# Optimization experiments

Measured on AMD Instinct MI355X. Metric: run time of the kernel, lower is better.

The kernel has to match this reference:

```python
import jax, jax.numpy as jnp
import numpy as np

N = 50000      # nodes
E = 800000     # edges
CIN = 128
CH = 128
COUT = 64
EPS = 1e-5     # BatchNorm eps


def setup_inputs() -> dict:
    key = jax.random.key(0)
    ks = jax.random.split(key, 16)
    s = 0.1  # weight scale for numerical stability
    return {
        "x": jax.random.normal(ks[0], (N, CIN), jnp.float32),
        "edge_index": jax.random.randint(ks[1], (2, E), 0, N, jnp.int32),
        "edge_weights": jax.random.uniform(ks[2], (E,), jnp.float32),
        "w1": jax.random.normal(ks[3], (CIN, CH), jnp.float32) * s,
        "b1": jnp.zeros((CH,), jnp.float32),
        "bn1_g": jnp.ones((CH,), jnp.float32),
        "bn1_b": jnp.zeros((CH,), jnp.float32),
        "bn1_m": jax.random.normal(ks[4], (CH,), jnp.float32) * 0.1,
        "bn1_v": jax.random.uniform(ks[5], (CH,), jnp.float32) + 0.5,
        "conv_ws": jax.random.normal(ks[6], (2, CH, CH), jnp.float32) * s,
        "conv_bs": jnp.zeros((2, CH), jnp.float32),
        "bns_g": jnp.ones((2, CH), jnp.float32),
        "bns_b": jnp.zeros((2, CH), jnp.float32),
        "bns_m": jax.random.normal(ks[7], (2, CH), jnp.float32) * 0.1,
        "bns_v": jax.random.uniform(ks[8], (2, CH), jnp.float32) + 0.5,
        "lin1_w": jax.random.normal(ks[9], (CH, CH), jnp.float32) * s,
        "lin1_b": jnp.zeros((CH,), jnp.float32),
        "lin2_w": jax.random.normal(ks[10], (CH, COUT), jnp.float32) * s,
        "lin2_b": jnp.zeros((COUT,), jnp.float32),
    }


def _bn(h, g, b, m, v):
    # BatchNorm1d in eval mode: running statistics
    return (h - m) * jax.lax.rsqrt(v + EPS) * g + b


def _gcn(h, w, b, src, dst, norm, n):
    # GCNConv: out[dst] += norm_e * (h @ W)[src]  (self loops already in src/dst)
    h = h @ w
    msg = h[src] * norm[:, None]                 # [E+N, CH]
    return jax.ops.segment_sum(msg, dst, num_segments=n) + b


def reference(x, edge_index, edge_weights, w1, b1, bn1_g, bn1_b, bn1_m, bn1_v,
              conv_ws, conv_bs, bns_g, bns_b, bns_m, bns_v,
              lin1_w, lin1_b, lin2_w, lin2_b):
    n = x.shape[0]
    loop = jnp.arange(n, dtype=edge_index.dtype)
    src = jnp.concatenate([edge_index[0], loop])
    dst = jnp.concatenate([edge_index[1], loop])
    ew = jnp.concatenate([edge_weights, jnp.ones((n,), edge_weights.dtype)])
    # symmetric degree normalization (PyG gcn_norm)
    deg = jax.ops.segment_sum(ew, dst, num_segments=n)
    dis = jnp.where(deg > 0, jax.lax.rsqrt(deg), 0.0)
    norm = dis[src] * ew * dis[dst]

    lrelu = jax.nn.leaky_relu  # slope 0.01, matches F.leaky_relu default
    h = lrelu(_bn(_gcn(x, w1, b1, src, dst, norm, n), bn1_g, bn1_b, bn1_m, bn1_v))
    for i in range(conv_ws.shape[0]):
        h = lrelu(_bn(_gcn(h, conv_ws[i], conv_bs[i], src, dst, norm, n),
                      bns_g[i], bns_b[i], bns_m[i], bns_v[i]) + h)
    h = lrelu(h @ lin1_w + lin1_b)
    # dropout is identity in eval mode
    return h @ lin2_w + lin2_b
```

## Files before the change

kernel.cpp:

```cpp
#include <hip/hip_runtime.h>
#include <hip/hip_bf16.h>


constexpr int   NN    = 50000;
constexpr int   EE    = 800000;
constexpr int   CH    = 128;
constexpr int   SLOTS = 64;
constexpr float EPS   = 1e-5f;

typedef __attribute__((ext_vector_type(8))) short bf16x8;
typedef __attribute__((ext_vector_type(4))) float f32x4;
typedef unsigned long long u64;
typedef unsigned short u16;

__device__ inline u16 f2bf_rne(float f) {
  unsigned u = __float_as_uint(f);
  unsigned r = u + 0x7fffu + ((u >> 16) & 1u);
  return (u16)(r >> 16);
}
__device__ inline float bf2f(unsigned h16) {
  return __uint_as_float(h16 << 16);
}


__global__ void init_kernel(unsigned* __restrict__ ell) {
  int i = blockIdx.x * blockDim.x + threadIdx.x;
  if (i < NN) ell[(size_t)i * SLOTS] = 1u;
}

__global__ void edge_kernel(const int* __restrict__ ei, const float* __restrict__ ew,
                            unsigned* __restrict__ ell) {
  int e = blockIdx.x * blockDim.x + threadIdx.x;
  if (e >= EE) return;
  int s = ei[e], d = ei[EE + e];
  float w = ew[e];
  unsigned rank = atomicAdd(&ell[(size_t)d * SLOTS], 1u);
  if (rank < SLOTS)
    ell[(size_t)d * SLOTS + rank] = ((unsigned)f2bf_rne(w) << 16) | (unsigned)s;
}

constexpr int NB_DIS = (NN * 16 + 255) / 256;
constexpr int NB_WZ  = (73728 + 255) / 256;

__global__ void prep_kernel(
    const unsigned* __restrict__ ell, float* __restrict__ dis,
    const float* __restrict__ w1, const float* __restrict__ bn1_g, const float* __restrict__ bn1_v,
    const float* __restrict__ conv_ws, const float* __restrict__ bns_g, const float* __restrict__ bns_v,
    const float* __restrict__ lin1_w, const float* __restrict__ lin2_w,
    u16* __restrict__ w1h, u16* __restrict__ w1l,
    u16* __restrict__ c0h, u16* __restrict__ c0l,
    u16* __restrict__ c1h, u16* __restrict__ c1l,
    u16* __restrict__ l1h, u16* __restrict__ l1l,
    u16* __restrict__ l2h, u16* __restrict__ l2l)
{
  if (blockIdx.x < NB_DIS) {
    int lane = threadIdx.x & 63;
    int sub  = lane & 15;
    int node = ((blockIdx.x * 256 + threadIdx.x) >> 6) * 4 + (lane >> 4);
    if (node >= NN) return;
    uint4 vv = *(const uint4*)(ell + (size_t)node * SLOTS + sub * 4);
    unsigned cnt = (unsigned)__shfl((int)vv.x, lane & 48);
    if (cnt > SLOTS) cnt = SLOTS;
    unsigned wv[4] = {vv.x, vv.y, vv.z, vv.w};
    float s = 0.f;
    #pragma unroll
    for (int q = 0; q < 4; q++) {
      int slot = sub * 4 + q;
      if (slot >= 1 && slot < (int)cnt) s += bf2f(wv[q] >> 16);
    }
    #pragma unroll
    for (int off = 1; off < 16; off <<= 1) s += __shfl_xor(s, off);
    if (sub == 0) dis[node] = rsqrtf(1.0f + s);
    return;
  }

  int idx = (blockIdx.x - NB_DIS) * 256 + threadIdx.x;
  const float* W; const float* g = nullptr; const float* v = nullptr;
  u16 *hi, *lo; int CO = 128; int local;
  if      (idx < 16384) { W = w1;              g = bn1_g;     v = bn1_v;     hi = w1h; lo = w1l; local = idx; }
  else if (idx < 32768) { W = conv_ws;         g = bns_g;     v = bns_v;     hi = c0h; lo = c0l; local = idx - 16384; }
  else if (idx < 49152) { W = conv_ws + 16384; g = bns_g+128; v = bns_v+128; hi = c1h; lo = c1l; local = idx - 32768; }
  else if (idx < 65536) { W = lin1_w;                                        hi = l1h; lo = l1l; local = idx - 49152; }
  else if (idx < 73728) { W = lin2_w;                                        hi = l2h; lo = l2l; local = idx - 65536; CO = 64; }
  else return;
  int k = local / CO, n = local % CO;
  float w = W[local];
  if (g) w *= g[n] * rsqrtf(v[n] + EPS);
  int NCT = CO / 16;
  int kchunk = k >> 5, kin = k & 31, quad = kin >> 3, j = kin & 7;
  int ct = n >> 4, l = (quad << 4) | (n & 15);
  size_t pos = ((size_t)(kchunk * NCT + ct) * 64 + l) * 8 + j;
  u16 h = f2bf_rne(w);
  hi[pos] = h;
  lo[pos] = f2bf_rne(w - bf2f(h));
}

template<int CO, int EPI, bool OUT_BF16, bool A_BF16, bool SCALE>
__global__ __launch_bounds__(256) void mgemm_kernel(
    const void* __restrict__ Ain,
    const u16* __restrict__ Whi, const u16* __restrict__ Wlo,
    const float* __restrict__ bias, const float* __restrict__ dis,
    void* __restrict__ Cout)
{
  constexpr int NCT = CO / 16;
  __shared__ float lds[64][CO + 4];

  const int tid  = threadIdx.x;
  const int wave = tid >> 6;
  const int lane = tid & 63;
  const int quad = lane >> 4;
  const int mrow = lane & 15;
  const int row0 = blockIdx.x * 64;

  int arow = row0 + wave * 16 + mrow;
  if (arow >= NN) arow = NN - 1;

  bf16x8 ahi[4], alo[4];
  if constexpr (A_BF16) {
    const u16* Ar = (const u16*)Ain + (size_t)arow * CH;
    #pragma unroll
    for (int c = 0; c < 4; c++)
      ahi[c] = *(const bf16x8*)(Ar + c * 32 + quad * 8);
  } else {
    const float* Ar = (const float*)Ain + (size_t)arow * CH;
    #pragma unroll
    for (int c = 0; c < 4; c++) {
      int off = c * 32 + quad * 8;
      float4 f0 = *(const float4*)(Ar + off);
      float4 f1 = *(const float4*)(Ar + off + 4);
      float f[8] = {f0.x, f0.y, f0.z, f0.w, f1.x, f1.y, f1.z, f1.w};
      #pragma unroll
      for (int j = 0; j < 8; j++) {
        u16 h = f2bf_rne(f[j]);
        ahi[c][j] = (short)h;
        alo[c][j] = (short)f2bf_rne(f[j] - bf2f(h));
      }
    }
  }

  f32x4 acc[NCT];
  #pragma unroll
  for (int t = 0; t < NCT; t++) acc[t] = (f32x4){0.f, 0.f, 0.f, 0.f};

  #pragma unroll
  for (int c = 0; c < 4; c++) {
    #pragma unroll
    for (int t = 0; t < NCT; t++) {
      size_t base = ((size_t)(c * NCT + t) * 64 + lane) * 8;
      bf16x8 bh = *(const bf16x8*)(Whi + base);
      bf16x8 bl = *(const bf16x8*)(Wlo + base);
      acc[t] = __builtin_amdgcn_mfma_f32_16x16x32_bf16(ahi[c], bh, acc[t], 0, 0, 0);
      if constexpr (!A_BF16)
        acc[t] = __builtin_amdgcn_mfma_f32_16x16x32_bf16(alo[c], bh, acc[t], 0, 0, 0);
      acc[t] = __builtin_amdgcn_mfma_f32_16x16x32_bf16(ahi[c], bl, acc[t], 0, 0, 0);
    }
  }

  #pragma unroll
  for (int t = 0; t < NCT; t++)
    #pragma unroll
    for (int r = 0; r < 4; r++)
      lds[wave * 16 + quad * 4 + r][t * 16 + mrow] = acc[t][r];
  __syncthreads();

  constexpr int TOTE = 64 * CO / 4;
  #pragma unroll
  for (int i = tid; i < TOTE; i += 256) {
    int row = (i * 4) / CO;
    int col = (i * 4) % CO;
    int grow = row0 + row;
    if (grow >= NN) continue;
    float rs = 1.0f;
    if constexpr (SCALE) rs = dis[grow];
    const float* lp = &lds[row][col];
    float o[4];
    #pragma unroll
    for (int q = 0; q < 4; q++) {
      float x = lp[q];
      if constexpr (EPI >= 1) {
        x += bias[col + q];
        if constexpr (EPI == 1) x = x > 0.f ? x : 0.01f * x;
      }
      if constexpr (SCALE) x *= rs;
      o[q] = x;
    }
    if constexpr (OUT_BF16) {
      u16* cp = (u16*)Cout + (size_t)grow * CO + col;
      unsigned p0 = ((unsigned)f2bf_rne(o[1]) << 16) | f2bf_rne(o[0]);
      unsigned p1 = ((unsigned)f2bf_rne(o[3]) << 16) | f2bf_rne(o[2]);
      *(uint2*)cp = make_uint2(p0, p1);
    } else {
      float* cp = (float*)Cout + (size_t)grow * CO + col;
      *(float4*)cp = make_float4(o[0], o[1], o[2], o[3]);
    }
  }
}

template<bool RES>
__global__ __launch_bounds__(256) void agg_kernel(
    const u16* __restrict__ hw,
    const unsigned* __restrict__ ell, const float* __restrict__ dis,
    const float* __restrict__ conv_b, const float* __restrict__ g,
    const float* __restrict__ bb, const float* __restrict__ m,
    const float* __restrict__ v,
    const u16* __restrict__ res, u16* __restrict__ out)
{
  int node = (blockIdx.x * blockDim.x + threadIdx.x) >> 6;
  int lane = threadIdx.x & 63;
  if (node >= NN) return;

  unsigned myword = ell[(size_t)node * SLOTS + lane];
  int cnt = __shfl((int)myword, 0);
  if (cnt > SLOTS) cnt = SLOTS;

  unsigned us = *(const unsigned*)(hw + (size_t)node * CH + lane * 2);
  float ax = bf2f(us & 0xffffu);
  float ay = bf2f(us >> 16);

  int j = 1;
  for (; j + 4 <= cnt; j += 4) {
    unsigned e0 = (unsigned)__shfl((int)myword, j);
    unsigned e1 = (unsigned)__shfl((int)myword, j + 1);
    unsigned e2 = (unsigned)__shfl((int)myword, j + 2);
    unsigned e3 = (unsigned)__shfl((int)myword, j + 3);
    unsigned u0 = *(const unsigned*)(hw + (size_t)(e0 & 0xffffu) * CH + lane * 2);
    unsigned u1 = *(const unsigned*)(hw + (size_t)(e1 & 0xffffu) * CH + lane * 2);
    unsigned u2 = *(const unsigned*)(hw + (size_t)(e2 & 0xffffu) * CH + lane * 2);
    unsigned u3 = *(const unsigned*)(hw + (size_t)(e3 & 0xffffu) * CH + lane * 2);
    float w0 = bf2f(e0 >> 16), w1 = bf2f(e1 >> 16);
    float w2 = bf2f(e2 >> 16), w3 = bf2f(e3 >> 16);
    ax = fmaf(w0, bf2f(u0 & 0xffffu), ax); ay = fmaf(w0, bf2f(u0 >> 16), ay);
    ax = fmaf(w1, bf2f(u1 & 0xffffu), ax); ay = fmaf(w1, bf2f(u1 >> 16), ay);
    ax = fmaf(w2, bf2f(u2 & 0xffffu), ax); ay = fmaf(w2, bf2f(u2 >> 16), ay);
    ax = fmaf(w3, bf2f(u3 & 0xffffu), ax); ay = fmaf(w3, bf2f(u3 >> 16), ay);
  }
  for (; j < cnt; j++) {
    unsigned e0 = (unsigned)__shfl((int)myword, j);
    unsigned u0 = *(const unsigned*)(hw + (size_t)(e0 & 0xffffu) * CH + lane * 2);
    float w0 = bf2f(e0 >> 16);
    ax = fmaf(w0, bf2f(u0 & 0xffffu), ax); ay = fmaf(w0, bf2f(u0 >> 16), ay);
  }

  float disd = dis[node];
  int c = lane * 2;
  float sc0 = g[c]     * rsqrtf(v[c]     + EPS);
  float sc1 = g[c + 1] * rsqrtf(v[c + 1] + EPS);
  float y0 = ax * disd + (conv_b[c]     - m[c])     * sc0 + bb[c];
  float y1 = ay * disd + (conv_b[c + 1] - m[c + 1]) * sc1 + bb[c + 1];
  if constexpr (RES) {
    unsigned r = *(const unsigned*)(res + (size_t)node * CH + c);
    y0 += bf2f(r & 0xffffu);
    y1 += bf2f(r >> 16);
  }
  y0 = y0 > 0.f ? y0 : 0.01f * y0;
  y1 = y1 > 0.f ? y1 : 0.01f * y1;
  *(unsigned*)(out + (size_t)node * CH + c) =
      ((unsigned)f2bf_rne(y1) << 16) | f2bf_rne(y0);
}


extern "C" void kernel_launch(void* const* d_in, const int* in_sizes, int n_in,
                              void* d_out, int out_size, void* d_ws, size_t ws_size,
                              hipStream_t stream) {
  const float* x       = (const float*)d_in[0];
  const int*   ei      = (const int*)  d_in[1];
  const float* ew      = (const float*)d_in[2];
  const float* w1      = (const float*)d_in[3];
  const float* b1      = (const float*)d_in[4];
  const float* bn1_g   = (const float*)d_in[5];
  const float* bn1_b   = (const float*)d_in[6];
  const float* bn1_m   = (const float*)d_in[7];
  const float* bn1_v   = (const float*)d_in[8];
  const float* conv_ws = (const float*)d_in[9];
  const float* conv_bs = (const float*)d_in[10];
  const float* bns_g   = (const float*)d_in[11];
  const float* bns_b   = (const float*)d_in[12];
  const float* bns_m   = (const float*)d_in[13];
  const float* bns_v   = (const float*)d_in[14];
  const float* lin1_w  = (const float*)d_in[15];
  const float* lin1_b  = (const float*)d_in[16];
  const float* lin2_w  = (const float*)d_in[17];
  const float* lin2_b  = (const float*)d_in[18];
  float* out = (float*)d_out;

  size_t off = 0;
  auto alloc = [&](size_t elems) -> void* {
    void* p = (char*)d_ws + off * 4;
    off += (elems + 3) & ~(size_t)3;
    return p;
  };
  unsigned* ell = (unsigned*)alloc((size_t)NN * SLOTS);
  float*    dis = (float*)   alloc(NN);
  u16*      hwb = (u16*)     alloc((size_t)NN * CH / 2);
  u16*      hA  = (u16*)     alloc((size_t)NN * CH / 2);
  u16* w1h = (u16*)alloc(CH * CH / 2); u16* w1l = (u16*)alloc(CH * CH / 2);
  u16* c0h = (u16*)alloc(CH * CH / 2); u16* c0l = (u16*)alloc(CH * CH / 2);
  u16* c1h = (u16*)alloc(CH * CH / 2); u16* c1l = (u16*)alloc(CH * CH / 2);
  u16* l1h = (u16*)alloc(CH * CH / 2); u16* l1l = (u16*)alloc(CH * CH / 2);
  u16* l2h = (u16*)alloc(CH * 64 / 2); u16* l2l = (u16*)alloc(CH * 64 / 2);

  const int nb_n    = (NN + 255) / 256;
  const int nb_e    = (EE + 255) / 256;
  const int nb_gemm = (NN + 63) / 64;
  const int nb_agg  = (NN * 64 + 255) / 256;
  dim3 B(256);

  init_kernel<<<nb_n, B, 0, stream>>>(ell);
  edge_kernel<<<nb_e, B, 0, stream>>>(ei, ew, ell);
  prep_kernel<<<NB_DIS + NB_WZ, B, 0, stream>>>(ell, dis,
      w1, bn1_g, bn1_v, conv_ws, bns_g, bns_v, lin1_w, lin2_w,
      w1h, w1l, c0h, c0l, c1h, c1l, l1h, l1l, l2h, l2l);

  mgemm_kernel<128, 0, true, false, true><<<nb_gemm, B, 0, stream>>>(x, w1h, w1l, nullptr, dis, hwb);
  agg_kernel<false><<<nb_agg, B, 0, stream>>>(hwb, ell, dis,
      b1, bn1_g, bn1_b, bn1_m, bn1_v, nullptr, hA);

  mgemm_kernel<128, 0, true, true, true><<<nb_gemm, B, 0, stream>>>(hA, c0h, c0l, nullptr, dis, hwb);
  agg_kernel<true><<<nb_agg, B, 0, stream>>>(hwb, ell, dis,
      conv_bs, bns_g, bns_b, bns_m, bns_v, hA, hA);

  mgemm_kernel<128, 0, true, true, true><<<nb_gemm, B, 0, stream>>>(hA, c1h, c1l, nullptr, dis, hwb);
  agg_kernel<true><<<nb_agg, B, 0, stream>>>(hwb, ell, dis,
      conv_bs + CH, bns_g + CH, bns_b + CH, bns_m + CH, bns_v + CH, hA, hA);

  mgemm_kernel<128, 1, true,  true, false><<<nb_gemm, B, 0, stream>>>(hA, l1h, l1l, lin1_b, nullptr, hwb);
  mgemm_kernel<64,  2, false, true, false><<<nb_gemm, B, 0, stream>>>(hwb, l2h, l2l, lin2_b, nullptr, out);
}
```

Measured before the change: 353.1 us.

## Bucket edges via two-pass LDS binning and fuse final two linear layers

Replaces the global-atomic ELL construction with a two-pass scheme. Edges are first binned by destination block of 64 nodes using shared-memory counters, then each bucket is scattered into the ELL rows with LDS atomics, and the degree normalization is computed in the same pass. The lin1 and lin2 GEMMs are fused into one kernel that keeps the intermediate activations in LDS, so the 50000x128 intermediate no longer makes a round trip through global memory. The cost is an extra bins buffer with fixed bucket capacity (RCAP), which could drop edges if a bucket overflows. It also changes rounding, since the intermediate stays fp32 and is split into hi and lo bf16 parts instead of being stored as bf16.

```diff
diff --git a/kernel.cpp b/kernel.cpp
--- a/kernel.cpp
+++ b/kernel.cpp
@@ -6,6 +6,9 @@
 constexpr int   EE    = 800000;
 constexpr int   CH    = 128;
 constexpr int   SLOTS = 64;
+constexpr int   NBUK  = 782;
+constexpr int   RCAP  = 2048;
+constexpr int   EPB   = 4096;
 constexpr float EPS   = 1e-5f;
 
 typedef __attribute__((ext_vector_type(8))) short bf16x8;
@@ -23,27 +26,82 @@
 }
 
 
-__global__ void init_kernel(unsigned* __restrict__ ell) {
-  int i = blockIdx.x * blockDim.x + threadIdx.x;
-  if (i < NN) ell[(size_t)i * SLOTS] = 1u;
-}
-
-__global__ void edge_kernel(const int* __restrict__ ei, const float* __restrict__ ew,
-                            unsigned* __restrict__ ell) {
-  int e = blockIdx.x * blockDim.x + threadIdx.x;
-  if (e >= EE) return;
-  int s = ei[e], d = ei[EE + e];
-  float w = ew[e];
-  unsigned rank = atomicAdd(&ell[(size_t)d * SLOTS], 1u);
-  if (rank < SLOTS)
-    ell[(size_t)d * SLOTS + rank] = ((unsigned)f2bf_rne(w) << 16) | (unsigned)s;
-}
-
-constexpr int NB_DIS = (NN * 16 + 255) / 256;
-constexpr int NB_WZ  = (73728 + 255) / 256;
-
-__global__ void prep_kernel(
-    const unsigned* __restrict__ ell, float* __restrict__ dis,
+__global__ __launch_bounds__(256) void bin_kernel(const int* __restrict__ ei,
+                                                  const float* __restrict__ ew,
+                                                  unsigned* __restrict__ gcur,
+                                                  u64* __restrict__ bins) {
+  __shared__ unsigned cnt[NBUK];
+  __shared__ unsigned base[NBUK];
+  const int tid = threadIdx.x;
+  for (int b = tid; b < NBUK; b += 256) cnt[b] = 0;
+  __syncthreads();
+  const int e0 = blockIdx.x * EPB;
+  unsigned pk[16]; u16 bkt[16]; u16 rnk[16]; unsigned char dl[16];
+  #pragma unroll
+  for (int i = 0; i < 16; i++) {
+    int e = e0 + i * 256 + tid;
+    if (e < EE) {
+      int s = ei[e], d = ei[EE + e];
+      float w = ew[e];
+      bkt[i] = (u16)(d >> 6);
+      dl[i]  = (unsigned char)(d & 63);
+      pk[i]  = ((unsigned)f2bf_rne(w) << 16) | (unsigned)s;
+      rnk[i] = (u16)atomicAdd(&cnt[bkt[i]], 1u);
+    } else bkt[i] = 0xffffu;
+  }
+  __syncthreads();
+  for (int b = tid; b < NBUK; b += 256) {
+    unsigned c = cnt[b];
+    base[b] = c ? atomicAdd(&gcur[b * 16], c) : 0u;
+  }
+  __syncthreads();
+  #pragma unroll
+  for (int i = 0; i < 16; i++) {
+    if (bkt[i] == 0xffffu) continue;
+    unsigned pos = base[bkt[i]] + rnk[i];
+    if (pos < RCAP)
+      bins[(size_t)bkt[i] * RCAP + pos] = ((u64)dl[i] << 32) | pk[i];
+  }
+}
+
+
+__global__ __launch_bounds__(256) void scatter_kernel(const unsigned* __restrict__ gcur,
+                                                      const u64* __restrict__ bins,
+                                                      unsigned* __restrict__ ell,
+                                                      float* __restrict__ dis) {
+  __shared__ unsigned rank[64];
+  __shared__ float    wsum[64];
+  const int b   = blockIdx.x;
+  const int tid = threadIdx.x;
+  if (tid < 64) { rank[tid] = 1u; wsum[tid] = 0.f; }
+  __syncthreads();
+  unsigned cnt = gcur[b * 16];
+  if (cnt > RCAP) cnt = RCAP;
+  const u64* src = bins + (size_t)b * RCAP;
+  for (unsigned i = tid; i < cnt; i += 256) {
+    u64 v = src[i];
+    unsigned pk = (unsigned)v;
+    unsigned dl = (unsigned)(v >> 32);
+    unsigned r = atomicAdd(&rank[dl], 1u);
+    if (r < SLOTS)
+      ell[((size_t)(b * 64 + dl)) * SLOTS + r] = pk;
+    atomicAdd(&wsum[dl], bf2f(pk >> 16));
+  }
+  __syncthreads();
+  if (tid < 64) {
+    int node = b * 64 + tid;
+    if (node < NN) {
+      unsigned c = rank[tid];
+      if (c > SLOTS) c = SLOTS;
+      ell[(size_t)node * SLOTS] = c;
+      dis[node] = rsqrtf(1.0f + wsum[tid]);
+    }
+  }
+}
+
+constexpr int NB_WZ = (73728 + 255) / 256;
+
+__global__ void wswz_kernel(
     const float* __restrict__ w1, const float* __restrict__ bn1_g, const float* __restrict__ bn1_v,
     const float* __restrict__ conv_ws, const float* __restrict__ bns_g, const float* __restrict__ bns_v,
     const float* __restrict__ lin1_w, const float* __restrict__ lin2_w,
@@ -53,28 +111,7 @@
     u16* __restrict__ l1h, u16* __restrict__ l1l,
     u16* __restrict__ l2h, u16* __restrict__ l2l)
 {
-  if (blockIdx.x < NB_DIS) {
-    int lane = threadIdx.x & 63;
-    int sub  = lane & 15;
-    int node = ((blockIdx.x * 256 + threadIdx.x) >> 6) * 4 + (lane >> 4);
-    if (node >= NN) return;
-    uint4 vv = *(const uint4*)(ell + (size_t)node * SLOTS + sub * 4);
-    unsigned cnt = (unsigned)__shfl((int)vv.x, lane & 48);
-    if (cnt > SLOTS) cnt = SLOTS;
-    unsigned wv[4] = {vv.x, vv.y, vv.z, vv.w};
-    float s = 0.f;
-    #pragma unroll
-    for (int q = 0; q < 4; q++) {
-      int slot = sub * 4 + q;
-      if (slot >= 1 && slot < (int)cnt) s += bf2f(wv[q] >> 16);
-    }
-    #pragma unroll
-    for (int off = 1; off < 16; off <<= 1) s += __shfl_xor(s, off);
-    if (sub == 0) dis[node] = rsqrtf(1.0f + s);
-    return;
-  }
-
-  int idx = (blockIdx.x - NB_DIS) * 256 + threadIdx.x;
+  int idx = blockIdx.x * 256 + threadIdx.x;
   const float* W; const float* g = nullptr; const float* v = nullptr;
   u16 *hi, *lo; int CO = 128; int local;
   if      (idx < 16384) { W = w1;              g = bn1_g;     v = bn1_v;     hi = w1h; lo = w1l; local = idx; }
@@ -192,6 +229,96 @@
     } else {
       float* cp = (float*)Cout + (size_t)grow * CO + col;
       *(float4*)cp = make_float4(o[0], o[1], o[2], o[3]);
+    }
+  }
+}
+
+__global__ __launch_bounds__(256) void linf_kernel(
+    const u16* __restrict__ Ain,
+    const u16* __restrict__ l1h, const u16* __restrict__ l1l,
+    const float* __restrict__ b1,
+    const u16* __restrict__ l2h, const u16* __restrict__ l2l,
+    const float* __restrict__ b2, float* __restrict__ out)
+{
+  __shared__ float lds[64][CH + 4];
+  const int tid  = threadIdx.x;
+  const int wave = tid >> 6;
+  const int lane = tid & 63;
+  const int quad = lane >> 4;
+  const int mrow = lane & 15;
+  const int row0 = blockIdx.x * 64;
+
+  int arow = row0 + wave * 16 + mrow;
+  if (arow >= NN) arow = NN - 1;
+
+  bf16x8 a1[4];
+  {
+    const u16* Ar = Ain + (size_t)arow * CH;
+    #pragma unroll
+    for (int c = 0; c < 4; c++)
+      a1[c] = *(const bf16x8*)(Ar + c * 32 + quad * 8);
+  }
+  f32x4 acc[8];
+  #pragma unroll
+  for (int t = 0; t < 8; t++) acc[t] = (f32x4){0.f, 0.f, 0.f, 0.f};
+  #pragma unroll
+  for (int c = 0; c < 4; c++) {
+    #pragma unroll
+    for (int t = 0; t < 8; t++) {
+      size_t base = ((size_t)(c * 8 + t) * 64 + lane) * 8;
+      bf16x8 bh = *(const bf16x8*)(l1h + base);
+      bf16x8 bl = *(const bf16x8*)(l1l + base);
+      acc[t] = __builtin_amdgcn_mfma_f32_16x16x32_bf16(a1[c], bh, acc[t], 0, 0, 0);
+      acc[t] = __builtin_amdgcn_mfma_f32_16x16x32_bf16(a1[c], bl, acc[t], 0, 0, 0);
+    }
+  }
+  #pragma unroll
+  for (int t = 0; t < 8; t++) {
+    float bb = b1[t * 16 + mrow];
+    #pragma unroll
+    for (int r = 0; r < 4; r++) {
+      float x = acc[t][r] + bb;
+      x = x > 0.f ? x : 0.01f * x;
+      lds[wave * 16 + quad * 4 + r][t * 16 + mrow] = x;
+    }
+  }
+  __syncthreads();
+
+  f32x4 acc2[4];
+  #pragma unroll
+  for (int t = 0; t < 4; t++) acc2[t] = (f32x4){0.f, 0.f, 0.f, 0.f};
+  const int lrow = wave * 16 + mrow;
+  #pragma unroll
+  for (int c = 0; c < 4; c++) {
+    bf16x8 ahi, alo;
+    const float* lp = &lds[lrow][c * 32 + quad * 8];
+    float4 f0 = *(const float4*)lp;
+    float4 f1 = *(const float4*)(lp + 4);
+    float f[8] = {f0.x, f0.y, f0.z, f0.w, f1.x, f1.y, f1.z, f1.w};
+    #pragma unroll
+    for (int j = 0; j < 8; j++) {
+      u16 h = f2bf_rne(f[j]);
+      ahi[j] = (short)h;
+      alo[j] = (short)f2bf_rne(f[j] - bf2f(h));
+    }
+    #pragma unroll
+    for (int t = 0; t < 4; t++) {
+      size_t base = ((size_t)(c * 4 + t) * 64 + lane) * 8;
+      bf16x8 bh = *(const bf16x8*)(l2h + base);
+      bf16x8 bl = *(const bf16x8*)(l2l + base);
+      acc2[t] = __builtin_amdgcn_mfma_f32_16x16x32_bf16(ahi, bh, acc2[t], 0, 0, 0);
+      acc2[t] = __builtin_amdgcn_mfma_f32_16x16x32_bf16(alo, bh, acc2[t], 0, 0, 0);
+      acc2[t] = __builtin_amdgcn_mfma_f32_16x16x32_bf16(ahi, bl, acc2[t], 0, 0, 0);
+    }
+  }
+  #pragma unroll
+  for (int t = 0; t < 4; t++) {
+    float bb = b2[t * 16 + mrow];
+    #pragma unroll
+    for (int r = 0; r < 4; r++) {
+      int grow = row0 + wave * 16 + quad * 4 + r;
+      if (grow < NN)
+        out[(size_t)grow * 64 + t * 16 + mrow] = acc2[t][r] + bb;
     }
   }
 }
@@ -289,27 +416,29 @@
     off += (elems + 3) & ~(size_t)3;
     return p;
   };
-  unsigned* ell = (unsigned*)alloc((size_t)NN * SLOTS);
-  float*    dis = (float*)   alloc(NN);
-  u16*      hwb = (u16*)     alloc((size_t)NN * CH / 2);
-  u16*      hA  = (u16*)     alloc((size_t)NN * CH / 2);
+  unsigned* gcur = (unsigned*)alloc(NBUK * 16);
+  u64*      bins = (u64*)     alloc((size_t)NBUK * RCAP * 2);
+  unsigned* ell  = (unsigned*)alloc((size_t)NN * SLOTS);
+  float*    dis  = (float*)   alloc(NN);
+  u16*      hwb  = (u16*)     alloc((size_t)NN * CH / 2);
+  u16*      hA   = (u16*)     alloc((size_t)NN * CH / 2);
   u16* w1h = (u16*)alloc(CH * CH / 2); u16* w1l = (u16*)alloc(CH * CH / 2);
   u16* c0h = (u16*)alloc(CH * CH / 2); u16* c0l = (u16*)alloc(CH * CH / 2);
   u16* c1h = (u16*)alloc(CH * CH / 2); u16* c1l = (u16*)alloc(CH * CH / 2);
   u16* l1h = (u16*)alloc(CH * CH / 2); u16* l1l = (u16*)alloc(CH * CH / 2);
   u16* l2h = (u16*)alloc(CH * 64 / 2); u16* l2l = (u16*)alloc(CH * 64 / 2);
 
-  const int nb_n    = (NN + 255) / 256;
-  const int nb_e    = (EE + 255) / 256;
+  const int nb_bin  = (EE + EPB - 1) / EPB;
   const int nb_gemm = (NN + 63) / 64;
   const int nb_agg  = (NN * 64 + 255) / 256;
   dim3 B(256);
 
-  init_kernel<<<nb_n, B, 0, stream>>>(ell);
-  edge_kernel<<<nb_e, B, 0, stream>>>(ei, ew, ell);
-  prep_kernel<<<NB_DIS + NB_WZ, B, 0, stream>>>(ell, dis,
-      w1, bn1_g, bn1_v, conv_ws, bns_g, bns_v, lin1_w, lin2_w,
-      w1h, w1l, c0h, c0l, c1h, c1l, l1h, l1l, l2h, l2l);
+  hipMemsetAsync(gcur, 0, NBUK * 16 * sizeof(unsigned), stream);
+  bin_kernel    <<<nb_bin, B, 0, stream>>>(ei, ew, gcur, bins);
+  scatter_kernel<<<NBUK,   B, 0, stream>>>(gcur, bins, ell, dis);
+
+  wswz_kernel<<<NB_WZ, B, 0, stream>>>(w1, bn1_g, bn1_v, conv_ws, bns_g, bns_v,
+      lin1_w, lin2_w, w1h, w1l, c0h, c0l, c1h, c1l, l1h, l1l, l2h, l2l);
 
   mgemm_kernel<128, 0, true, false, true><<<nb_gemm, B, 0, stream>>>(x, w1h, w1l, nullptr, dis, hwb);
   agg_kernel<false><<<nb_agg, B, 0, stream>>>(hwb, ell, dis,
@@ -323,6 +452,5 @@
   agg_kernel<true><<<nb_agg, B, 0, stream>>>(hwb, ell, dis,
       conv_bs + CH, bns_g + CH, bns_b + CH, bns_m + CH, bns_v + CH, hA, hA);
 
-  mgemm_kernel<128, 1, true,  true, false><<<nb_gemm, B, 0, stream>>>(hA, l1h, l1l, lin1_b, nullptr, hwb);
-  mgemm_kernel<64,  2, false, true, false><<<nb_gemm, B, 0, stream>>>(hwb, l2h, l2l, lin2_b, nullptr, out);
-}
+  linf_kernel<<<nb_gemm, B, 0, stream>>>(hA, l1h, l1l, lin1_b, l2h, l2l, lin2_b, out);
+}
```

Result: faster. 329.3 us (-6.8%).
